# Performance work log

Measured on AMD Instinct MI355X. Metric: run time of the kernel, lower is better.

The kernel has to match this reference:

```python
import jax, jax.numpy as jnp
import numpy as np
from math import ceil, log2


def _bizinter_real(x):
    # upsample-by-2 with zero insertion, then low-pass via FFT masking (torch _bizinter_real)
    N = x.shape[-1]
    u = jnp.stack([x, jnp.zeros_like(x)], axis=-1).reshape(x.shape[:-1] + (2 * N,))
    xf = jnp.fft.fft(u, axis=-1)
    N1 = N // 2 + N % 2
    N2 = 2 * N - N // 2
    idx = jnp.arange(2 * N)
    keep = (idx < N1) | (idx >= N2)
    xf = jnp.where(keep, xf, 0)
    return 2.0 * jnp.real(jnp.fft.ifft(xf, axis=-1))


def _corefrmod2(signal, a):
    # chirp-z style fractional Fourier core; signal length M is even here (M = 4N)
    M = signal.shape[-1]
    deltax = jnp.sqrt(jnp.asarray(M, jnp.float32))
    phi = a * jnp.pi / 2
    alpha = -1j * jnp.pi * jnp.tan(phi / 2)
    beta = 1j * jnp.pi / jnp.sin(phi)
    Aphi = jnp.exp(-1j * (jnp.pi * jnp.sign(jnp.sin(phi)) / 4 - phi / 2)) / jnp.sqrt(jnp.abs(jnp.sin(phi)))
    xg = jnp.arange(-(M % 2 + M // 2), M // 2) / deltax          # [M]
    chirp = jnp.exp(alpha * xg ** 2)                              # complex64 [M]
    multip = signal * chirp                                       # [..., M]
    t = jnp.arange(-M + 1, M) / deltax                            # [2M-1]
    hlptc = jnp.exp(beta * t ** 2)
    n2 = 2 ** int(ceil(log2(3 * M - 2)))                          # static pad length
    Hc = jnp.fft.ifft(jnp.fft.fft(multip, n=n2, axis=-1) * jnp.fft.fft(hlptc, n=n2), axis=-1)
    Hc = Hc[..., M - 1:2 * M - 1]                                 # valid part of linear conv
    return Hc * (Aphi * chirp) / deltax                           # M even -> no roll


def frft(x, a):
    # order a is in (0.5, 1.5) (normalized), so pre-modulation branches are skipped
    N = x.shape[-1]
    biz = _bizinter_real(x)                                       # [..., 2N]
    z = jnp.zeros(x.shape[:-1] + (N,), x.dtype)
    fc = jnp.concatenate([z, biz, z], axis=-1)                    # [..., 4N]
    res = _corefrmod2(fc, a)
    res = res[..., N:3 * N:2]                                     # index_select N..3N-1 then bizdec
    return res.at[..., 0].multiply(2.0)                           # double first entry


def setup_inputs() -> dict:
    key = jax.random.key(0)
    x = jax.random.normal(key, (128, 4096), dtype=jnp.float32)
    order = jnp.asarray(0.8, dtype=jnp.float32)                   # learned FrFT order parameter
    return {"x": x, "order": order}


def reference(x, order):
    return frft(x, order)
```

## Files before the change

### kernel.cpp

```cpp
#include <hip/hip_runtime.h>
#include <math.h>

#ifndef M_PI
#define M_PI 3.14159265358979323846
#endif

#define ROWS 128
#define NN   4096

#define TW_OFF   0
#define CA_OFF   65536
#define GEIN_OFF 131072
#define GOIN_OFF 196608
#define GE_OFF   262144
#define GO_OFF   327680
#define SC_OFF   393216

__device__ __forceinline__ int swz(int i) { return i ^ ((i >> 5) & 31); }

__device__ __forceinline__ int drev6(int v) {
    unsigned r = __brev((unsigned)v) >> 20;
    return (int)(((r & 0x555u) << 1) | ((r & 0xAAAu) >> 1));
}

template<int INV>
__device__ __forceinline__ void r2_8192(float* re, float* im,
                                        const float2* __restrict__ tw, int tid) {
    __syncthreads();
#pragma unroll
    for (int it = 0; it < 4; ++it) {
        const int n = tid + it * 1024;
        const int i0 = swz(n), i1 = swz(n + 4096);
        const float ur = re[i0], ui = im[i0];
        const float vr = re[i1], vi = im[i1];
        const float2 w = tw[n];
        const float wi = INV ? -w.y : w.y;
        if (!INV) {
            const float dr = ur - vr, di = ui - vi;
            re[i0] = ur + vr;            im[i0] = ui + vi;
            re[i1] = dr * w.x - di * wi; im[i1] = dr * wi + di * w.x;
        } else {
            const float br = vr * w.x - vi * wi, bi = vr * wi + vi * w.x;
            re[i0] = ur + br; im[i0] = ui + bi;
            re[i1] = ur - br; im[i1] = ui - bi;
        }
    }
}

template<int INV, int LS>
__device__ __forceinline__ void r4_stage(float* re, float* im,
                                         const float2* __restrict__ tw, int tid) {
    __syncthreads();
    const int Q = 1 << (LS - 2);
    const int TS = 13 - LS;
#pragma unroll
    for (int it = 0; it < 2; ++it) {
        const int gi = tid + it * 1024;
        const int q  = gi & (Q - 1);
        const int base = ((gi >> (LS - 2)) << LS) | q;
        const int i0 = swz(base), i1 = swz(base + Q), i2 = swz(base + 2 * Q), i3 = swz(base + 3 * Q);
        float ar = re[i0], ai = im[i0];
        float br = re[i1], bi = im[i1];
        float cr = re[i2], ci = im[i2];
        float dr = re[i3], di = im[i3];
        const float2 w1 = tw[q << TS];
        const float2 w2 = tw[(2 * q) << TS];
        const float2 w3 = tw[(3 * q) << TS];
        const float w1i = INV ? -w1.y : w1.y;
        const float w2i = INV ? -w2.y : w2.y;
        const float w3i = INV ? -w3.y : w3.y;
        if (!INV) {
            const float t0r = ar + cr, t0i = ai + ci;
            const float t1r = ar - cr, t1i = ai - ci;
            const float t2r = br + dr, t2i = bi + di;
            const float t3r = br - dr, t3i = bi - di;
            re[i0] = t0r + t2r; im[i0] = t0i + t2i;
            const float y1r = t1r + t3i, y1i = t1i - t3r;
            re[i1] = y1r * w1.x - y1i * w1i; im[i1] = y1r * w1i + y1i * w1.x;
            const float y2r = t0r - t2r, y2i = t0i - t2i;
            re[i2] = y2r * w2.x - y2i * w2i; im[i2] = y2r * w2i + y2i * w2.x;
            const float y3r = t1r - t3i, y3i = t1i + t3r;
            re[i3] = y3r * w3.x - y3i * w3i; im[i3] = y3r * w3i + y3i * w3.x;
        } else {
            const float b1r = br * w1.x - bi * w1i, b1i = br * w1i + bi * w1.x;
            const float b2r = cr * w2.x - ci * w2i, b2i = cr * w2i + ci * w2.x;
            const float b3r = dr * w3.x - di * w3i, b3i = dr * w3i + di * w3.x;
            const float s0r = ar + b2r, s0i = ai + b2i;
            const float s1r = ar - b2r, s1i = ai - b2i;
            const float s2r = b1r + b3r, s2i = b1i + b3i;
            const float s3r = b1r - b3r, s3i = b1i - b3i;
            re[i0] = s0r + s2r; im[i0] = s0i + s2i;
            re[i1] = s1r - s3i; im[i1] = s1i + s3r;
            re[i2] = s0r - s2r; im[i2] = s0i - s2i;
            re[i3] = s1r + s3i; im[i3] = s1i - s3r;
        }
    }
}

__device__ __forceinline__ void dif8192(float* re, float* im,
                                        const float2* __restrict__ tw, int tid) {
    r2_8192<0>(re, im, tw, tid);
    r4_stage<0, 12>(re, im, tw, tid);
    r4_stage<0, 10>(re, im, tw, tid);
    r4_stage<0, 8>(re, im, tw, tid);
    r4_stage<0, 6>(re, im, tw, tid);
    r4_stage<0, 4>(re, im, tw, tid);
    r4_stage<0, 2>(re, im, tw, tid);
}

__device__ __forceinline__ void dit8192(float* re, float* im,
                                        const float2* __restrict__ tw, int tid) {
    r4_stage<1, 2>(re, im, tw, tid);
    r4_stage<1, 4>(re, im, tw, tid);
    r4_stage<1, 6>(re, im, tw, tid);
    r4_stage<1, 8>(re, im, tw, tid);
    r4_stage<1, 10>(re, im, tw, tid);
    r4_stage<1, 12>(re, im, tw, tid);
    r2_8192<1>(re, im, tw, tid);
}

__global__ __launch_bounds__(256) void build_tables_k(const float* __restrict__ order,
                                                      char* __restrict__ ws) {
    const int gid  = blockIdx.x * 256 + threadIdx.x;
    const int nthr = gridDim.x * 256;
    const double a    = (double)order[0];
    const double phi  = a * (M_PI * 0.5);
    const double sp   = sin(phi);
    const double alph = -M_PI * tan(phi * 0.5);
    const double beta = M_PI / sp;
    float2* tw   = (float2*)(ws + TW_OFF);
    float2* cA   = (float2*)(ws + CA_OFF);
    float2* gein = (float2*)(ws + GEIN_OFF);
    float2* goin = (float2*)(ws + GOIN_OFF);
    float2* sc   = (float2*)(ws + SC_OFF);
    for (int k = gid; k < 8192; k += nthr) {
        double th = -2.0 * M_PI * (double)k / 8192.0;
        tw[k] = make_float2((float)cos(th), (float)sin(th));
    }
    for (int m = gid; m < 8192; m += nthr) {
        double xg = (double)(m - 4096) * (1.0 / 128.0);
        double th = alph * xg * xg;
        cA[m] = make_float2((float)cos(th), (float)sin(th));
    }
    for (int q = gid; q < 8192; q += nthr) {
        double de = (q < 4096) ? (double)(2 * q) : (double)(2 * q - 16384);
        double u  = de * (1.0 / 128.0);
        double te = beta * u * u;
        gein[q] = make_float2((float)cos(te), (float)sin(te));
        double dl = (q < 4096) ? (double)(2 * q - 1) : (double)(2 * q - 16385);
        double v  = dl * (1.0 / 128.0);
        double to = beta * v * v;
        goin[q] = make_float2((float)cos(to), (float)sin(to));
    }
    if (gid == 0) {
        double sgn = (sp >= 0.0) ? 1.0 : -1.0;
        double ang = -(M_PI * sgn * 0.25 - phi * 0.5);
        double amp = 1.0 / sqrt(fabs(sp));
        sc[0] = make_float2((float)(cos(ang) * amp / 128.0),
                            (float)(sin(ang) * amp / 128.0));
    }
}

__global__ __launch_bounds__(1024) void g_fft_k(char* __restrict__ ws) {
    __shared__ float re[8192];
    __shared__ float im[8192];
    const float2* tw  = (const float2*)(ws + TW_OFF);
    const float2* src = (const float2*)(ws + (blockIdx.x == 0 ? GEIN_OFF : GOIN_OFF));
    float2*       dst = (float2*)      (ws + (blockIdx.x == 0 ? GE_OFF   : GO_OFF));
    const int t = threadIdx.x;
#pragma unroll
    for (int j = 0; j < 8; ++j) {
        const int i = t + 1024 * j;
        const float2 v = src[i];
        re[swz(i)] = v.x; im[swz(i)] = v.y;
    }
    dif8192(re, im, tw, t);
    __syncthreads();
#pragma unroll
    for (int j = 0; j < 8; ++j) {
        const int i = t + 1024 * j;
        dst[i] = make_float2(re[swz(i)], im[swz(i)]);
    }
}

__global__ __launch_bounds__(1024) void row_k(const float* __restrict__ x,
                                              const char* __restrict__ ws,
                                              float* __restrict__ out,
                                              int write_complex) {
    __shared__ float re[8192];
    __shared__ float im[8192];
    const float2* tw = (const float2*)(ws + TW_OFF);
    const float2* cA = (const float2*)(ws + CA_OFF);
    const float2* GE = (const float2*)(ws + GE_OFF);
    const float2* GO = (const float2*)(ws + GO_OFF);
    const float2  sc = *(const float2*)(ws + SC_OFF);
    const int row = blockIdx.x;
    const int t   = threadIdx.x;

#pragma unroll
    for (int j = 0; j < 4; ++j) {
        const int i = t + 1024 * j;
        const float v = x[row * NN + i];
        re[swz(2 * i)] = v;      im[swz(2 * i)] = 0.f;
        re[swz(2 * i + 1)] = 0.f; im[swz(2 * i + 1)] = 0.f;
    }

    dif8192(re, im, tw, t);

    __syncthreads();
    const float s2 = 2.0f / 8192.0f;
#pragma unroll
    for (int j = 0; j < 8; ++j) {
        const int p = t + 1024 * j;
        const int d = drev6(p & 4095);
        const float f = (d < 1024 || d >= 3072) ? s2 : 0.f;
        const int idx = swz(p);
        re[idx] *= f; im[idx] *= f;
    }

    dit8192(re, im, tw, t);

    __syncthreads();
    float wer[4], wei[4], wor[4], woi[4];
#pragma unroll
    for (int j = 0; j < 4; ++j) {
        const int q = t + 1024 * j;
        const float be = re[swz(2 * q)];
        const float bo = re[swz(2 * q + 1)];
        const float2 ce = cA[2 * q];
        const float2 co = cA[2 * q + 1];
        wer[j] = be * ce.x; wei[j] = be * ce.y;
        wor[j] = bo * co.x; woi[j] = bo * co.y;
    }
    __syncthreads();
#pragma unroll
    for (int j = 0; j < 4; ++j) {
        const int q = t + 1024 * j;
        re[swz(q)] = wer[j];          im[swz(q)] = wei[j];
        re[swz(q + 4096)] = 0.f;      im[swz(q + 4096)] = 0.f;
    }

    dif8192(re, im, tw, t);

    __syncthreads();
    float yer[8], yei[8];
#pragma unroll
    for (int j = 0; j < 8; ++j) {
        const int p = t + 1024 * j;
        const int idx = swz(p);
        const float2 g = GE[p];
        const float wr = re[idx], wi_ = im[idx];
        yer[j] = wr * g.x - wi_ * g.y;
        yei[j] = wr * g.y + wi_ * g.x;
    }

    __syncthreads();
#pragma unroll
    for (int j = 0; j < 4; ++j) {
        const int q = t + 1024 * j;
        re[swz(q)] = wor[j];          im[swz(q)] = woi[j];
        re[swz(q + 4096)] = 0.f;      im[swz(q + 4096)] = 0.f;
    }

    dif8192(re, im, tw, t);

    __syncthreads();
#pragma unroll
    for (int j = 0; j < 8; ++j) {
        const int p = t + 1024 * j;
        const int idx = swz(p);
        const float2 g = GO[p];
        const float wr = re[idx], wi_ = im[idx];
        re[idx] = yer[j] + wr * g.x - wi_ * g.y;
        im[idx] = yei[j] + wr * g.y + wi_ * g.x;
    }

    dit8192(re, im, tw, t);

    __syncthreads();
    const float is = 1.0f / 8192.0f;
#pragma unroll
    for (int j = 0; j < 4; ++j) {
        const int o = t + 1024 * j;
        const int idx = swz(o);
        const float vr = re[idx] * is, vi = im[idx] * is;
        const float2 c = cA[2 * o];
        const float tr = vr * c.x - vi * c.y;
        const float ti = vr * c.y + vi * c.x;
        float rr = tr * sc.x - ti * sc.y;
        float ri = tr * sc.y + ti * sc.x;
        if (o == 0) { rr *= 2.f; ri *= 2.f; }
        const int gi = row * NN + o;
        if (write_complex) { out[2 * gi] = rr; out[2 * gi + 1] = ri; }
        else               { out[gi] = rr; }
    }
}

extern "C" void kernel_launch(void* const* d_in, const int* in_sizes, int n_in,
                              void* d_out, int out_size, void* d_ws, size_t ws_size,
                              hipStream_t stream) {
    const float* x     = (const float*)d_in[0];
    const float* order = (const float*)d_in[1];
    float* out = (float*)d_out;
    char*  ws  = (char*)d_ws;
    const int write_complex = (out_size >= 2 * ROWS * NN) ? 1 : 0;

    hipLaunchKernelGGL(build_tables_k, dim3(64), dim3(256), 0, stream, order, ws);
    hipLaunchKernelGGL(g_fft_k, dim3(2), dim3(1024), 0, stream, ws);
    hipLaunchKernelGGL(row_k, dim3(ROWS), dim3(1024), 0, stream, x, ws, out, write_complex);
}
```

Baseline: 131.3 us.

## Fuse kernel-FFT blocks into row kernel and shrink FFTs using signal structure

Merges the two chirp-filter FFT blocks into the main kernel as extra blocks and signals completion through global flags. Row blocks spin on those flags only after their own forward FFTs. The upsampling step becomes a 4096-point real FFT with a half-length inverse via a precomputed twiddle table, replacing two full 8192-point transforms. The zero-padded halves of the convolution FFTs are pre-twiddled so the first radix-2 stage is skipped, and the final inverse radix-2 is folded into the output step. Together this removes a launch and many FFT stages, but adds a cross-block spin-wait whose forward progress depends on the extra blocks being scheduled. It also moves the 1/8192 scaling into the filter tables.

```diff
diff --git a/kernel.cpp b/kernel.cpp
--- a/kernel.cpp
+++ b/kernel.cpp
@@ -7,6 +7,7 @@
 
 #define ROWS 128
 #define NN   4096
+#define MAGIC 0x13572468u
 
 #define TW_OFF   0
 #define CA_OFF   65536
@@ -15,12 +16,18 @@
 #define GE_OFF   262144
 #define GO_OFF   327680
 #define SC_OFF   393216
+#define FLAG_OFF 393224
+#define GT_OFF   458752
 
 __device__ __forceinline__ int swz(int i) { return i ^ ((i >> 5) & 31); }
 
 __device__ __forceinline__ int drev6(int v) {
     unsigned r = __brev((unsigned)v) >> 20;
     return (int)(((r & 0x555u) << 1) | ((r & 0xAAAu) >> 1));
+}
+
+__device__ __forceinline__ float2 cmul(float2 a, float2 b) {
+    return make_float2(a.x * b.x - a.y * b.y, a.x * b.y + a.y * b.x);
 }
 
 template<int INV>
@@ -47,14 +54,14 @@
     }
 }
 
-template<int INV, int LS>
+template<int INV, int LS, int NITER>
 __device__ __forceinline__ void r4_stage(float* re, float* im,
                                          const float2* __restrict__ tw, int tid) {
     __syncthreads();
     const int Q = 1 << (LS - 2);
     const int TS = 13 - LS;
 #pragma unroll
-    for (int it = 0; it < 2; ++it) {
+    for (int it = 0; it < NITER; ++it) {
         const int gi = tid + it * 1024;
         const int q  = gi & (Q - 1);
         const int base = ((gi >> (LS - 2)) << LS) | q;
@@ -97,28 +104,6 @@
     }
 }
 
-__device__ __forceinline__ void dif8192(float* re, float* im,
-                                        const float2* __restrict__ tw, int tid) {
-    r2_8192<0>(re, im, tw, tid);
-    r4_stage<0, 12>(re, im, tw, tid);
-    r4_stage<0, 10>(re, im, tw, tid);
-    r4_stage<0, 8>(re, im, tw, tid);
-    r4_stage<0, 6>(re, im, tw, tid);
-    r4_stage<0, 4>(re, im, tw, tid);
-    r4_stage<0, 2>(re, im, tw, tid);
-}
-
-__device__ __forceinline__ void dit8192(float* re, float* im,
-                                        const float2* __restrict__ tw, int tid) {
-    r4_stage<1, 2>(re, im, tw, tid);
-    r4_stage<1, 4>(re, im, tw, tid);
-    r4_stage<1, 6>(re, im, tw, tid);
-    r4_stage<1, 8>(re, im, tw, tid);
-    r4_stage<1, 10>(re, im, tw, tid);
-    r4_stage<1, 12>(re, im, tw, tid);
-    r2_8192<1>(re, im, tw, tid);
-}
-
 __global__ __launch_bounds__(256) void build_tables_k(const float* __restrict__ order,
                                                       char* __restrict__ ws) {
     const int gid  = blockIdx.x * 256 + threadIdx.x;
@@ -133,6 +118,7 @@
     float2* gein = (float2*)(ws + GEIN_OFF);
     float2* goin = (float2*)(ws + GOIN_OFF);
     float2* sc   = (float2*)(ws + SC_OFF);
+    float2* Gt   = (float2*)(ws + GT_OFF);
     for (int k = gid; k < 8192; k += nthr) {
         double th = -2.0 * M_PI * (double)k / 8192.0;
         tw[k] = make_float2((float)cos(th), (float)sin(th));
@@ -142,15 +128,22 @@
         double th = alph * xg * xg;
         cA[m] = make_float2((float)cos(th), (float)sin(th));
     }
+    const double gs = 1.0 / 8192.0;
     for (int q = gid; q < 8192; q += nthr) {
         double de = (q < 4096) ? (double)(2 * q) : (double)(2 * q - 16384);
         double u  = de * (1.0 / 128.0);
         double te = beta * u * u;
-        gein[q] = make_float2((float)cos(te), (float)sin(te));
+        gein[q] = make_float2((float)(cos(te) * gs), (float)(sin(te) * gs));
         double dl = (q < 4096) ? (double)(2 * q - 1) : (double)(2 * q - 16385);
         double v  = dl * (1.0 / 128.0);
         double to = beta * v * v;
-        goin[q] = make_float2((float)cos(to), (float)sin(to));
+        goin[q] = make_float2((float)(cos(to) * gs), (float)(sin(to) * gs));
+    }
+    for (int p = gid; p < 4096; p += nthr) {
+        const int j = drev6(p);
+        double th = M_PI * (double)j / 4096.0;
+        double ss = (j < 2048) ? (1.0 / 4096.0) : (-1.0 / 4096.0);
+        Gt[p] = make_float2((float)(cos(th) * ss), (float)(sin(th) * ss));
     }
     if (gid == 0) {
         double sgn = (sp >= 0.0) ? 1.0 : -1.0;
@@ -161,88 +154,142 @@
     }
 }
 
-__global__ __launch_bounds__(1024) void g_fft_k(char* __restrict__ ws) {
-    __shared__ float re[8192];
-    __shared__ float im[8192];
-    const float2* tw  = (const float2*)(ws + TW_OFF);
-    const float2* src = (const float2*)(ws + (blockIdx.x == 0 ? GEIN_OFF : GOIN_OFF));
-    float2*       dst = (float2*)      (ws + (blockIdx.x == 0 ? GE_OFF   : GO_OFF));
-    const int t = threadIdx.x;
-#pragma unroll
-    for (int j = 0; j < 8; ++j) {
-        const int i = t + 1024 * j;
-        const float2 v = src[i];
-        re[swz(i)] = v.x; im[swz(i)] = v.y;
-    }
-    dif8192(re, im, tw, t);
-    __syncthreads();
-#pragma unroll
-    for (int j = 0; j < 8; ++j) {
-        const int i = t + 1024 * j;
-        dst[i] = make_float2(re[swz(i)], im[swz(i)]);
-    }
-}
-
-__global__ __launch_bounds__(1024) void row_k(const float* __restrict__ x,
-                                              const char* __restrict__ ws,
-                                              float* __restrict__ out,
-                                              int write_complex) {
+__global__ __launch_bounds__(1024) void main_k(const float* __restrict__ x,
+                                               char* __restrict__ ws,
+                                               float* __restrict__ out,
+                                               int write_complex) {
     __shared__ float re[8192];
     __shared__ float im[8192];
     const float2* tw = (const float2*)(ws + TW_OFF);
+    const int t = threadIdx.x;
+    unsigned* flags = (unsigned*)(ws + FLAG_OFF);
+
+    if (blockIdx.x >= ROWS) {
+        const int kb = (int)blockIdx.x - ROWS;
+        const float2* src = (const float2*)(ws + (kb == 0 ? GEIN_OFF : GOIN_OFF));
+        float2*       dst = (float2*)      (ws + (kb == 0 ? GE_OFF   : GO_OFF));
+#pragma unroll
+        for (int j = 0; j < 8; ++j) {
+            const int i = t + 1024 * j;
+            const float2 v = src[i];
+            re[swz(i)] = v.x; im[swz(i)] = v.y;
+        }
+        r2_8192<0>(re, im, tw, t);
+        r4_stage<0, 12, 2>(re, im, tw, t);
+        r4_stage<0, 10, 2>(re, im, tw, t);
+        r4_stage<0,  8, 2>(re, im, tw, t);
+        r4_stage<0,  6, 2>(re, im, tw, t);
+        r4_stage<0,  4, 2>(re, im, tw, t);
+        r4_stage<0,  2, 2>(re, im, tw, t);
+        __syncthreads();
+#pragma unroll
+        for (int j = 0; j < 8; ++j) {
+            const int i = t + 1024 * j;
+            dst[i] = make_float2(re[swz(i)], im[swz(i)]);
+        }
+        __syncthreads();
+        __threadfence();
+        if (t == 0) atomicExch(&flags[kb], MAGIC);
+        return;
+    }
+
     const float2* cA = (const float2*)(ws + CA_OFF);
     const float2* GE = (const float2*)(ws + GE_OFF);
     const float2* GO = (const float2*)(ws + GO_OFF);
+    const float2* Gt = (const float2*)(ws + GT_OFF);
     const float2  sc = *(const float2*)(ws + SC_OFF);
     const int row = blockIdx.x;
-    const int t   = threadIdx.x;
-
-#pragma unroll
-    for (int j = 0; j < 4; ++j) {
-        const int i = t + 1024 * j;
-        const float v = x[row * NN + i];
-        re[swz(2 * i)] = v;      im[swz(2 * i)] = 0.f;
-        re[swz(2 * i + 1)] = 0.f; im[swz(2 * i + 1)] = 0.f;
-    }
-
-    dif8192(re, im, tw, t);
-
-    __syncthreads();
-    const float s2 = 2.0f / 8192.0f;
-#pragma unroll
-    for (int j = 0; j < 8; ++j) {
-        const int p = t + 1024 * j;
-        const int d = drev6(p & 4095);
-        const float f = (d < 1024 || d >= 3072) ? s2 : 0.f;
-        const int idx = swz(p);
-        re[idx] *= f; im[idx] *= f;
-    }
-
-    dit8192(re, im, tw, t);
-
-    __syncthreads();
-    float wer[4], wei[4], wor[4], woi[4];
-#pragma unroll
-    for (int j = 0; j < 4; ++j) {
-        const int q = t + 1024 * j;
-        const float be = re[swz(2 * q)];
-        const float bo = re[swz(2 * q + 1)];
+
+    float xr[4];
+#pragma unroll
+    for (int c = 0; c < 4; ++c) {
+        const int i = t + 1024 * c;
+        xr[c] = x[row * NN + i];
+        re[swz(i)] = xr[c]; im[swz(i)] = 0.f;
+    }
+
+    r4_stage<0, 12, 1>(re, im, tw, t);
+    r4_stage<0, 10, 1>(re, im, tw, t);
+    r4_stage<0,  8, 1>(re, im, tw, t);
+    r4_stage<0,  6, 1>(re, im, tw, t);
+    r4_stage<0,  4, 1>(re, im, tw, t);
+    r4_stage<0,  2, 1>(re, im, tw, t);
+
+    __syncthreads();
+    {
+        const int base = t << 2;
+        float vr[4], vi[4];
+#pragma unroll
+        for (int c = 0; c < 4; ++c) {
+            const int idx = swz(base + c);
+            const float2 g = Gt[base + c];
+            const float wr = re[idx], wi_ = im[idx];
+            vr[c] = wr * g.x - wi_ * g.y;
+            vi[c] = wr * g.y + wi_ * g.x;
+        }
+        const float s0r = vr[0] + vr[2], s0i = vi[0] + vi[2];
+        const float s1r = vr[0] - vr[2], s1i = vi[0] - vi[2];
+        const float s2r = vr[1] + vr[3], s2i = vi[1] + vi[3];
+        const float s3r = vr[1] - vr[3], s3i = vi[1] - vi[3];
+        re[swz(base)]     = s0r + s2r; im[swz(base)]     = s0i + s2i;
+        re[swz(base + 1)] = s1r - s3i; im[swz(base + 1)] = s1i + s3r;
+        re[swz(base + 2)] = s0r - s2r; im[swz(base + 2)] = s0i - s2i;
+        re[swz(base + 3)] = s1r + s3i; im[swz(base + 3)] = s1i - s3r;
+    }
+    r4_stage<1,  4, 1>(re, im, tw, t);
+    r4_stage<1,  6, 1>(re, im, tw, t);
+    r4_stage<1,  8, 1>(re, im, tw, t);
+    r4_stage<1, 10, 1>(re, im, tw, t);
+
+    float bo[4];
+    __syncthreads();
+    {
+        const int q = t;
+        const float ar = re[swz(t)],        ai = im[swz(t)];
+        const float br = re[swz(t + 1024)], bi = im[swz(t + 1024)];
+        const float cr = re[swz(t + 2048)], ci = im[swz(t + 2048)];
+        const float dr = re[swz(t + 3072)], di = im[swz(t + 3072)];
+        const float2 w1 = tw[q << 1];
+        const float2 w2 = tw[(2 * q) << 1];
+        const float2 w3 = tw[(3 * q) << 1];
+        const float b1r = br * w1.x + bi * w1.y, b1i = bi * w1.x - br * w1.y;
+        const float b2r = cr * w2.x + ci * w2.y, b2i = ci * w2.x - cr * w2.y;
+        const float b3r = dr * w3.x + di * w3.y, b3i = di * w3.x - dr * w3.y;
+        const float s0r = ar + b2r;
+        const float s1r = ar - b2r;
+        const float s2r = b1r + b3r;
+        const float s3i = b1i - b3i;
+        bo[0] = s0r + s2r;
+        bo[1] = s1r - s3i;
+        bo[2] = s0r - s2r;
+        bo[3] = s1r + s3i;
+    }
+    __syncthreads();
+
+#pragma unroll
+    for (int c = 0; c < 4; ++c) {
+        const int q = t + 1024 * c;
         const float2 ce = cA[2 * q];
-        const float2 co = cA[2 * q + 1];
-        wer[j] = be * ce.x; wei[j] = be * ce.y;
-        wor[j] = bo * co.x; woi[j] = bo * co.y;
-    }
-    __syncthreads();
-#pragma unroll
-    for (int j = 0; j < 4; ++j) {
-        const int q = t + 1024 * j;
-        re[swz(q)] = wer[j];          im[swz(q)] = wei[j];
-        re[swz(q + 4096)] = 0.f;      im[swz(q + 4096)] = 0.f;
-    }
-
-    dif8192(re, im, tw, t);
-
-    __syncthreads();
+        const float wr = xr[c] * ce.x, wi_ = xr[c] * ce.y;
+        const float2 w = tw[q];
+        re[swz(q)] = wr;          im[swz(q)] = wi_;
+        re[swz(q + 4096)] = wr * w.x - wi_ * w.y;
+        im[swz(q + 4096)] = wr * w.y + wi_ * w.x;
+    }
+    r4_stage<0, 12, 2>(re, im, tw, t);
+    r4_stage<0, 10, 2>(re, im, tw, t);
+    r4_stage<0,  8, 2>(re, im, tw, t);
+    r4_stage<0,  6, 2>(re, im, tw, t);
+    r4_stage<0,  4, 2>(re, im, tw, t);
+    r4_stage<0,  2, 2>(re, im, tw, t);
+
+    if (t == 0) {
+        while (atomicCAS(&flags[0], 0u, 0u) != MAGIC) {}
+        while (atomicCAS(&flags[1], 0u, 0u) != MAGIC) {}
+    }
+    __syncthreads();
+    __threadfence();
+
     float yer[8], yei[8];
 #pragma unroll
     for (int j = 0; j < 8; ++j) {
@@ -253,16 +300,22 @@
         yer[j] = wr * g.x - wi_ * g.y;
         yei[j] = wr * g.y + wi_ * g.x;
     }
-
-    __syncthreads();
-#pragma unroll
-    for (int j = 0; j < 4; ++j) {
-        const int q = t + 1024 * j;
-        re[swz(q)] = wor[j];          im[swz(q)] = woi[j];
-        re[swz(q + 4096)] = 0.f;      im[swz(q + 4096)] = 0.f;
-    }
-
-    dif8192(re, im, tw, t);
+#pragma unroll
+    for (int c = 0; c < 4; ++c) {
+        const int q = t + 1024 * c;
+        const float2 co = cA[2 * q + 1];
+        const float wr = bo[c] * co.x, wi_ = bo[c] * co.y;
+        const float2 w = tw[q];
+        re[swz(q)] = wr;          im[swz(q)] = wi_;
+        re[swz(q + 4096)] = wr * w.x - wi_ * w.y;
+        im[swz(q + 4096)] = wr * w.y + wi_ * w.x;
+    }
+    r4_stage<0, 12, 2>(re, im, tw, t);
+    r4_stage<0, 10, 2>(re, im, tw, t);
+    r4_stage<0,  8, 2>(re, im, tw, t);
+    r4_stage<0,  6, 2>(re, im, tw, t);
+    r4_stage<0,  4, 2>(re, im, tw, t);
+    r4_stage<0,  2, 2>(re, im, tw, t);
 
     __syncthreads();
 #pragma unroll
@@ -275,18 +328,26 @@
         im[idx] = yei[j] + wr * g.y + wi_ * g.x;
     }
 
-    dit8192(re, im, tw, t);
-
-    __syncthreads();
-    const float is = 1.0f / 8192.0f;
-#pragma unroll
-    for (int j = 0; j < 4; ++j) {
-        const int o = t + 1024 * j;
-        const int idx = swz(o);
-        const float vr = re[idx] * is, vi = im[idx] * is;
-        const float2 c = cA[2 * o];
-        const float tr = vr * c.x - vi * c.y;
-        const float ti = vr * c.y + vi * c.x;
+    r4_stage<1,  2, 2>(re, im, tw, t);
+    r4_stage<1,  4, 2>(re, im, tw, t);
+    r4_stage<1,  6, 2>(re, im, tw, t);
+    r4_stage<1,  8, 2>(re, im, tw, t);
+    r4_stage<1, 10, 2>(re, im, tw, t);
+    r4_stage<1, 12, 2>(re, im, tw, t);
+
+    __syncthreads();
+#pragma unroll
+    for (int c = 0; c < 4; ++c) {
+        const int o = t + 1024 * c;
+        const float ur = re[swz(o)],        ui = im[swz(o)];
+        const float vr = re[swz(o + 4096)], vi = im[swz(o + 4096)];
+        const float2 w = tw[o];
+        const float br = vr * w.x + vi * w.y;
+        const float bi = vi * w.x - vr * w.y;
+        const float yr = ur + br, yi = ui + bi;
+        const float2 cc = cA[2 * o];
+        const float tr = yr * cc.x - yi * cc.y;
+        const float ti = yr * cc.y + yi * cc.x;
         float rr = tr * sc.x - ti * sc.y;
         float ri = tr * sc.y + ti * sc.x;
         if (o == 0) { rr *= 2.f; ri *= 2.f; }
@@ -306,6 +367,6 @@
     const int write_complex = (out_size >= 2 * ROWS * NN) ? 1 : 0;
 
     hipLaunchKernelGGL(build_tables_k, dim3(64), dim3(256), 0, stream, order, ws);
-    hipLaunchKernelGGL(g_fft_k, dim3(2), dim3(1024), 0, stream, ws);
-    hipLaunchKernelGGL(row_k, dim3(ROWS), dim3(1024), 0, stream, x, ws, out, write_complex);
-}
+    hipLaunchKernelGGL(main_k, dim3(ROWS + 2), dim3(1024), 0, stream,
+                       x, ws, out, write_complex);
+}
```

After: 170.1 us. +29.6%, slower.
